# Optimization experiments

Measured on AMD Instinct MI355X. Metric: run time of the kernel, lower is better.

Reference implementation:

```python
import jax, jax.numpy as jnp
import numpy as np

B, N, D = 32, 540, 512
H = 8
DH = D // H
MAX_LEN = 540
POS_CLIP = MAX_LEN - 1


def setup_inputs() -> dict:
    key = jax.random.key(0)
    ks = jax.random.split(key, 12)
    s = 0.02
    inp = {
        "query": jax.random.normal(ks[0], (B, N, D), dtype=jnp.float32),
        "Wq": jax.random.normal(ks[1], (D, D), dtype=jnp.float32) * s,
        "bq": jnp.zeros((D,), jnp.float32),
        "Wk": jax.random.normal(ks[2], (D, D), dtype=jnp.float32) * s,
        "bk": jnp.zeros((D,), jnp.float32),
        "Wv": jax.random.normal(ks[3], (D, D), dtype=jnp.float32) * s,
        "bv": jnp.zeros((D,), jnp.float32),
        "Wh": jax.random.normal(ks[4], (D, D), dtype=jnp.float32) * s,
        "bh": jnp.zeros((D,), jnp.float32),
        "pos_k": jax.random.uniform(ks[5], (2 * POS_CLIP + 1, DH), dtype=jnp.float32, minval=-0.05, maxval=0.05),
        "gamma": jnp.ones((D,), jnp.float32),
        "beta": jnp.zeros((D,), jnp.float32),
        "valid_len": jax.random.randint(ks[6], (B,), 1, N + 1, dtype=jnp.int32),
    }
    return inp


def _split_heads(x):
    # [B, N, D] -> [H*B, N, DH], head-major on axis 0 (matches tf.concat(tf.split(x,H,-1),0))
    return x.reshape(B, N, H, DH).transpose(2, 0, 1, 3).reshape(H * B, N, DH)


def reference(query, Wq, bq, Wk, bk, Wv, bv, Wh, bh, pos_k, gamma, beta, valid_len):
    q = _split_heads(query @ Wq + bq)  # [HB, N, DH]
    k = _split_heads(query @ Wk + bk)
    v = _split_heads(query @ Wv + bv)

    QK = jnp.einsum("xqd,xkd->xqk", q, k)  # [HB, N, N]

    # relative position bias (Shaw et al. 2018)
    rel = jnp.arange(N)[None, :] - jnp.arange(N)[:, None]
    rel = jnp.clip(rel, -POS_CLIP, POS_CLIP) + POS_CLIP
    pos_enc_k = pos_k[rel]  # [N, N, DH]
    QR = jnp.einsum("xqd,qkd->xqk", q, pos_enc_k)

    attn = (QK + QR) / jnp.sqrt(jnp.float32(DH))

    # key-side sequence mask, broadcast over heads and query rows
    key_mask = jnp.arange(N)[None, :] < valid_len[:, None]  # [B, N]
    key_mask = jnp.tile(key_mask[:, None, :], (H, N, 1))  # [HB, N, N]
    attn = jnp.where(key_mask, attn, jnp.float32(-1e12))
    attn = jax.nn.softmax(attn, axis=-1)

    out = jnp.einsum("xqk,xkd->xqd", attn, v)  # [HB, N, DH]
    out = out.reshape(H, B, N, DH).transpose(1, 2, 0, 3).reshape(B, N, D)
    out = out @ Wh + bh
    out = out + query

    # layer norm over last axis
    mean = jnp.mean(out, axis=-1, keepdims=True)
    var = jnp.mean(jnp.square(out - mean), axis=-1, keepdims=True)
    normalized = (out - mean) * jax.lax.rsqrt(var + 1e-7)
    return gamma * normalized + beta
```

## Files before the change

kernel.cpp:

```cpp
#include <hip/hip_runtime.h>
#include <hip/hip_bf16.h>

typedef __hip_bfloat16 bf16;

#define NB 32
#define NSEQ 540
#define ND 512
#define NH 8
#define NDH 64
#define NHB 256
#define NM 17280
#define NPOS 1079
#define VTP 544

typedef __bf16 v8bf __attribute__((ext_vector_type(8)));
typedef float f32x4 __attribute__((ext_vector_type(4)));

union U8 {
  uint4 u;
  unsigned short s[8];
  v8bf v;
};

__device__ __forceinline__ unsigned short f2b(float x) {
  union { float f; unsigned u; } c;
  c.f = x;
  const unsigned r = c.u + 0x7fffu + ((c.u >> 16) & 1u);
  return (unsigned short)(r >> 16);
}

__device__ __forceinline__ float b2f16(unsigned short s) {
  return __uint_as_float(((unsigned)s) << 16);
}

__device__ __forceinline__ void cvt16(const float* __restrict__ p,
                                      unsigned short* __restrict__ dst) {
  unsigned short s[16];
#pragma unroll
  for (int i = 0; i < 4; i++) {
    const float4 v = *(const float4*)(p + i * 4);
    s[i * 4 + 0] = f2b(v.x);
    s[i * 4 + 1] = f2b(v.y);
    s[i * 4 + 2] = f2b(v.z);
    s[i * 4 + 3] = f2b(v.w);
  }
  *(uint4*)dst = *(uint4*)s;
  *(uint4*)(dst + 8) = *(uint4*)(s + 8);
}

__global__ __launch_bounds__(256) void pos_cvt(const float* __restrict__ pos,
                                              unsigned short* __restrict__ posb) {
  const int i = blockIdx.x * 256 + threadIdx.x;
  if (i < NPOS * NDH) posb[i] = f2b(pos[i]);
}

__global__ __launch_bounds__(256) void xcvt(const float* __restrict__ x,
                                            unsigned short* __restrict__ xb) {
  const int i = blockIdx.x * 256 + threadIdx.x;
  const float4 a = *(const float4*)(x + (size_t)i * 8);
  const float4 b = *(const float4*)(x + (size_t)i * 8 + 4);
  unsigned short s[8];
  s[0] = f2b(a.x); s[1] = f2b(a.y); s[2] = f2b(a.z); s[3] = f2b(a.w);
  s[4] = f2b(b.x); s[5] = f2b(b.y); s[6] = f2b(b.z); s[7] = f2b(b.w);
  *(uint4*)(xb + (size_t)i * 8) = *(uint4*)s;
}

__global__ __launch_bounds__(256) void wcvt(
    const float* __restrict__ Wq, const float* __restrict__ Wk,
    const float* __restrict__ Wv, const float* __restrict__ Wh,
    unsigned short* __restrict__ Wt) {
  __shared__ unsigned short T[64][72];
  const int tid = threadIdx.x;
  const int sel = blockIdx.z;
  const float* W = (sel == 0) ? Wq : (sel == 1) ? Wk : (sel == 2) ? Wv : Wh;
  unsigned short* out = Wt + (size_t)sel * ND * ND;
  const int k0 = blockIdx.x * 64, n0 = blockIdx.y * 64;
  const int r = tid >> 2, g = tid & 3;
  cvt16(W + (size_t)(k0 + r) * ND + n0 + g * 16, &T[r][g * 16]);
  __syncthreads();
  unsigned short s[16];
#pragma unroll
  for (int j = 0; j < 16; j++) s[j] = T[g * 16 + j][r];
  unsigned short* dst = out + (size_t)(n0 + r) * ND + k0 + g * 16;
  *(uint4*)dst = *(uint4*)s;
  *(uint4*)(dst + 8) = *(uint4*)(s + 8);
}

#define GEMM_MFMA_TAIL                                                            \
    __syncthreads();                                                              \
    U8 af[4], bfr[4];                                                             \
    _Pragma("unroll")                                                             \
    for (int mi = 0; mi < 4; mi++)                                                \
      af[mi].u = *(const uint4*)&As[wr * 64 + mi * 16 + l15][quad * 8];           \
    _Pragma("unroll")                                                             \
    for (int ni = 0; ni < 4; ni++)                                                \
      bfr[ni].u = *(const uint4*)&Bs[wc * 64 + ni * 16 + l15][quad * 8];          \
    _Pragma("unroll")                                                             \
    for (int mi = 0; mi < 4; mi++)                                                \
      _Pragma("unroll")                                                           \
      for (int ni = 0; ni < 4; ni++)                                              \
        acc[mi][ni] = __builtin_amdgcn_mfma_f32_16x16x32_bf16(                    \
            af[mi].v, bfr[ni].v, acc[mi][ni], 0, 0, 0);

#define GEMM_CORE_B16(APTR)                                                       \
  for (int k0 = 0; k0 < 512; k0 += 32) {                                          \
    __syncthreads();                                                              \
    {                                                                             \
      const unsigned short* apb = APTR + (size_t)(m0 + srow) * ND + k0 + sh;      \
      *(uint4*)&As[srow][sh] = *(const uint4*)apb;                                \
      *(uint4*)&As[srow][sh + 8] = *(const uint4*)(apb + 8);                      \
      const unsigned short* bp = Bt + (size_t)(n0 + srow) * ND + k0 + sh;         \
      *(uint4*)&Bs[srow][sh] = *(const uint4*)bp;                                 \
      *(uint4*)&Bs[srow][sh + 8] = *(const uint4*)(bp + 8);                       \
    }                                                                             \
    GEMM_MFMA_TAIL                                                                \
  }

#define GEMM_CORE_F32(APTR)                                                       \
  for (int k0 = 0; k0 < 512; k0 += 32) {                                          \
    __syncthreads();                                                              \
    cvt16(APTR + (size_t)(m0 + srow) * ND + k0 + sh, &As[srow][sh]);              \
    {                                                                             \
      const unsigned short* bp = Bt + (size_t)(n0 + srow) * ND + k0 + sh;         \
      *(uint4*)&Bs[srow][sh] = *(const uint4*)bp;                                 \
      *(uint4*)&Bs[srow][sh + 8] = *(const uint4*)(bp + 8);                       \
    }                                                                             \
    GEMM_MFMA_TAIL                                                                \
  }

__global__ __launch_bounds__(256, 3) void qkv_mfma(
    const unsigned short* __restrict__ Xb, const unsigned short* __restrict__ Wt,
    const float* __restrict__ bq, const float* __restrict__ bk,
    const float* __restrict__ bv,
    bf16* __restrict__ qh, bf16* __restrict__ kh, bf16* __restrict__ vt) {
  __shared__ unsigned short As[128][40];
  __shared__ unsigned short Bs[128][40];
  const int tid = threadIdx.x;
  const int sel = blockIdx.z;
  const unsigned short* Bt = Wt + (size_t)sel * ND * ND;
  const float* bias = (sel == 0) ? bq : (sel == 1) ? bk : bv;
  const int m0 = blockIdx.y * 128, n0 = blockIdx.x * 128;
  const int lane = tid & 63, w = tid >> 6;
  const int wr = w & 1, wc = w >> 1;
  const int l15 = lane & 15, quad = lane >> 4;
  const int srow = tid >> 1, sh = (tid & 1) * 16;

  f32x4 acc[4][4];
#pragma unroll
  for (int mi = 0; mi < 4; mi++)
#pragma unroll
    for (int ni = 0; ni < 4; ni++) acc[mi][ni] = (f32x4){0.f, 0.f, 0.f, 0.f};

  GEMM_CORE_B16(Xb)

  if (sel != 2) {
    unsigned short* o = (unsigned short*)((sel == 0) ? qh : kh);
#pragma unroll
    for (int mi = 0; mi < 4; mi++) {
      const int m = m0 + wr * 64 + mi * 16 + quad * 4;
      const int bidx = m / NSEQ;
      const int seq0 = m - bidx * NSEQ;
#pragma unroll
      for (int ni = 0; ni < 4; ni++) {
        const int n = n0 + wc * 64 + ni * 16 + l15;
        const int h = n >> 6, dh = n & 63;
        const float bsv = bias[n];
        const size_t base = (((size_t)(h * NB + bidx)) * NSEQ + seq0) * NDH + dh;
#pragma unroll
        for (int i = 0; i < 4; i++)
          o[base + (size_t)i * NDH] = f2b(acc[mi][ni][i] + bsv);
      }
    }
  } else {
    unsigned short* o = (unsigned short*)vt;
#pragma unroll
    for (int mi = 0; mi < 4; mi++) {
      const int m = m0 + wr * 64 + mi * 16 + quad * 4;
      const int bidx = m / NSEQ;
      const int seq0 = m - bidx * NSEQ;
#pragma unroll
      for (int ni = 0; ni < 4; ni++) {
        const int n = n0 + wc * 64 + ni * 16 + l15;
        const int h = n >> 6, dh = n & 63;
        const float bsv = bias[n];
        unsigned short pk[4];
#pragma unroll
        for (int i = 0; i < 4; i++) pk[i] = f2b(acc[mi][ni][i] + bsv);
        *(uint2*)(o + (((size_t)(h * NB + bidx)) * NDH + dh) * VTP + seq0) =
            *(uint2*)pk;
      }
    }
  }
}

__global__ __launch_bounds__(256, 3) void out_mfma(
    const float* __restrict__ ctx, const unsigned short* __restrict__ Wht,
    const float* __restrict__ bh, const float* __restrict__ query,
    float* __restrict__ tmp) {
  __shared__ unsigned short As[128][40];
  __shared__ unsigned short Bs[128][40];
  const int tid = threadIdx.x;
  const unsigned short* Bt = Wht;
  const int m0 = blockIdx.y * 128, n0 = blockIdx.x * 128;
  const int lane = tid & 63, w = tid >> 6;
  const int wr = w & 1, wc = w >> 1;
  const int l15 = lane & 15, quad = lane >> 4;
  const int srow = tid >> 1, sh = (tid & 1) * 16;

  f32x4 acc[4][4];
#pragma unroll
  for (int mi = 0; mi < 4; mi++)
#pragma unroll
    for (int ni = 0; ni < 4; ni++) acc[mi][ni] = (f32x4){0.f, 0.f, 0.f, 0.f};

  GEMM_CORE_F32(ctx)

#pragma unroll
  for (int mi = 0; mi < 4; mi++) {
    const int m = m0 + wr * 64 + mi * 16 + quad * 4;
#pragma unroll
    for (int ni = 0; ni < 4; ni++) {
      const int n = n0 + wc * 64 + ni * 16 + l15;
      const float bsv = bh[n];
#pragma unroll
      for (int i = 0; i < 4; i++) {
        const size_t off = (size_t)(m + i) * ND + n;
        tmp[off] = acc[mi][ni][i] + bsv + query[off];
      }
    }
  }
}

#define PW 584

__global__ __launch_bounds__(256, 5) void attn(
    const bf16* __restrict__ qh, const bf16* __restrict__ kh,
    const bf16* __restrict__ vt, const unsigned short* __restrict__ posb,
    const int* __restrict__ vlen, float* __restrict__ ctx) {
  __shared__ unsigned short P[16][PW];
  __shared__ float Tt[2][16][84];
  __shared__ float red4[16][4];
  __shared__ float sinv[16];

  const int tid = threadIdx.x;
  const int lane = tid & 63;
  const int w = tid >> 6;
  const int l15 = lane & 15;
  const int quad = lane >> 4;
  const int qb = blockIdx.x;
  const int x = blockIdx.y;
  const int b = x & 31, h = x >> 5;
  const int q0 = qb * 16;
  const int valid = vlen[b];
  const int NT = (valid + 63) >> 6;
  const int NC = (valid + 31) >> 5;
  const bf16* qbase = qh + (size_t)x * NSEQ * NDH;
  const unsigned short* kbase = (const unsigned short*)(kh + (size_t)x * NSEQ * NDH);
  const unsigned short* vbase = (const unsigned short*)(vt + (size_t)x * NDH * VTP);

  U8 aq0, aq1;
  {
    const int q = q0 + l15;
    if (q < NSEQ) {
      aq0.u = *(const uint4*)(qbase + (size_t)q * NDH + quad * 8);
      aq1.u = *(const uint4*)(qbase + (size_t)q * NDH + 32 + quad * 8);
    } else {
      aq0.u = make_uint4(0, 0, 0, 0);
      aq1.u = make_uint4(0, 0, 0, 0);
    }
  }

  U8 ck0, ck1, cp0, cp1, ce0, ce1;
  {
    const int key = w * 16 + l15;
    ck0.u = *(const uint4*)(kbase + (size_t)key * NDH + quad * 8);
    ck1.u = *(const uint4*)(kbase + (size_t)key * NDH + 32 + quad * 8);
    const long pr = (long)(524 - q0 + w * 16 + l15);
    cp0.u = *(const uint4*)(posb + pr * NDH + quad * 8);
    cp1.u = *(const uint4*)(posb + pr * NDH + 32 + quad * 8);
    if (w == 0) {
      const long pr2 = (long)(524 - q0 + 64 + l15);
      ce0.u = *(const uint4*)(posb + pr2 * NDH + quad * 8);
      ce1.u = *(const uint4*)(posb + pr2 * NDH + 32 + quad * 8);
    }
  }

  float pmax[4];
#pragma unroll
  for (int i = 0; i < 4; i++) pmax[i] = -1e30f;

  for (int kt = 0; kt < NT; kt++) {
    const int buf = kt & 1;
    U8 nk0, nk1, np0, np1, ne0, ne1;
    if (kt < NT - 1) {
      const int k1 = kt * 64 + 64;
      const int key = k1 + w * 16 + l15;
      nk0.u = *(const uint4*)(kbase + (size_t)key * NDH + quad * 8);
      nk1.u = *(const uint4*)(kbase + (size_t)key * NDH + 32 + quad * 8);
      const long pr = (long)(k1 - q0 + 524 + w * 16 + l15);
      np0.u = *(const uint4*)(posb + pr * NDH + quad * 8);
      np1.u = *(const uint4*)(posb + pr * NDH + 32 + quad * 8);
      if (w == 0) {
        const long pr2 = (long)(k1 - q0 + 524 + 64 + l15);
        ne0.u = *(const uint4*)(posb + pr2 * NDH + quad * 8);
        ne1.u = *(const uint4*)(posb + pr2 * NDH + 32 + quad * 8);
      }
    }

    f32x4 accqk = {0.f, 0.f, 0.f, 0.f};
    accqk = __builtin_amdgcn_mfma_f32_16x16x32_bf16(aq0.v, ck0.v, accqk, 0, 0, 0);
    accqk = __builtin_amdgcn_mfma_f32_16x16x32_bf16(aq1.v, ck1.v, accqk, 0, 0, 0);
    {
      f32x4 accT = {0.f, 0.f, 0.f, 0.f};
      accT = __builtin_amdgcn_mfma_f32_16x16x32_bf16(aq0.v, cp0.v, accT, 0, 0, 0);
      accT = __builtin_amdgcn_mfma_f32_16x16x32_bf16(aq1.v, cp1.v, accT, 0, 0, 0);
#pragma unroll
      for (int i = 0; i < 4; i++) Tt[buf][quad * 4 + i][w * 16 + l15] = accT[i];
      if (w == 0) {
        f32x4 accT2 = {0.f, 0.f, 0.f, 0.f};
        accT2 = __builtin_amdgcn_mfma_f32_16x16x32_bf16(aq0.v, ce0.v, accT2, 0, 0, 0);
        accT2 = __builtin_amdgcn_mfma_f32_16x16x32_bf16(aq1.v, ce1.v, accT2, 0, 0, 0);
#pragma unroll
        for (int i = 0; i < 4; i++) Tt[buf][quad * 4 + i][64 + l15] = accT2[i];
      }
    }
    __syncthreads();
    {
      const int k0 = kt * 64;
      const int kk = w * 16 + l15;
      const bool cm = (k0 + kk) < valid;
#pragma unroll
      for (int i = 0; i < 4; i++) {
        const int qq = quad * 4 + i;
        const float v = (accqk[i] + Tt[buf][qq][kk + 15 - qq]) * 0.125f;
        P[qq][k0 + kk] = f2b(v);
        if (cm) pmax[i] = fmaxf(pmax[i], v);
      }
    }
    ck0 = nk0; ck1 = nk1; cp0 = np0; cp1 = np1;
    if (w == 0) { ce0 = ne0; ce1 = ne1; }
  }

#pragma unroll
  for (int m = 1; m < 16; m <<= 1) {
#pragma unroll
    for (int i = 0; i < 4; i++)
      pmax[i] = fmaxf(pmax[i], __shfl_xor(pmax[i], m, 16));
  }
  if (l15 == 0) {
#pragma unroll
    for (int i = 0; i < 4; i++) red4[quad * 4 + i][w] = pmax[i];
  }

  const int dh = w * 16 + l15;
  const unsigned short* vrow = vbase + (size_t)dh * VTP;
  U8 cv;
  cv.u = *(const uint4*)(vrow + quad * 8);

  __syncthreads();

  {
    const int r = tid >> 4, c = tid & 15;
    const float4 rm = *(const float4*)red4[r];
    const float rowmax = fmaxf(fmaxf(rm.x, rm.y), fmaxf(rm.z, rm.w));
    const int nv = (valid + 7) >> 3;
    float sl = 0.f;
    for (int ch = c; ch < nv; ch += 16) {
      const uint4 u = *(const uint4*)&P[r][ch * 8];
      unsigned ue[4];
#pragma unroll
      for (int jj = 0; jj < 4; jj++) {
        const unsigned uu = ((const unsigned*)&u)[jj];
        const float lo = __uint_as_float(uu << 16);
        const float hi = __uint_as_float(uu & 0xffff0000u);
        float el = __expf(lo - rowmax);
        float eh = __expf(hi - rowmax);
        const int cb = ch * 8 + jj * 2;
        el = (cb < valid) ? el : 0.f;
        eh = (cb + 1 < valid) ? eh : 0.f;
        sl += el + eh;
        ue[jj] = (unsigned)f2b(el) | ((unsigned)f2b(eh) << 16);
      }
      *(uint4*)&P[r][ch * 8] = *(const uint4*)ue;
    }
    for (int ch = c; ch < 72; ch += 16) {
      if (ch >= nv) *(uint4*)&P[r][ch * 8] = make_uint4(0, 0, 0, 0);
    }
#pragma unroll
    for (int m = 1; m < 16; m <<= 1) sl += __shfl_xor(sl, m, 16);
    if (c == 0) sinv[r] = 1.f / sl;
  }
  __syncthreads();

  f32x4 acco = {0.f, 0.f, 0.f, 0.f};
  for (int ci = 0; ci < NC; ci++) {
    U8 nv_;
    if (ci + 1 < NC) nv_.u = *(const uint4*)(vrow + (ci + 1) * 32 + quad * 8);
    U8 ap;
    ap.u = *(const uint4*)&P[l15][ci * 32 + quad * 8];
    acco = __builtin_amdgcn_mfma_f32_16x16x32_bf16(ap.v, cv.v, acco, 0, 0, 0);
    cv = nv_;
  }
#pragma unroll
  for (int i = 0; i < 4; i++) {
    const int q = q0 + quad * 4 + i;
    if (q < NSEQ) {
      ctx[((size_t)b * NSEQ + q) * ND + h * NDH + dh] = acco[i] * sinv[quad * 4 + i];
    }
  }
}

__global__ __launch_bounds__(256) void lnorm(
    const float* __restrict__ tmp, const float* __restrict__ gamma,
    const float* __restrict__ beta, float* __restrict__ out) {
  __shared__ float sred[256];
  const int row = blockIdx.x;
  const int tid = threadIdx.x;
  const size_t base = (size_t)row * 512;
  const float x0 = tmp[base + tid];
  const float x1 = tmp[base + 256 + tid];

  sred[tid] = x0 + x1;
  __syncthreads();
  for (int o = 128; o > 0; o >>= 1) {
    if (tid < o) sred[tid] += sred[tid + o];
    __syncthreads();
  }
  const float mean = sred[0] * (1.f / 512.f);
  __syncthreads();
  const float d0 = x0 - mean, d1 = x1 - mean;
  sred[tid] = d0 * d0 + d1 * d1;
  __syncthreads();
  for (int o = 128; o > 0; o >>= 1) {
    if (tid < o) sred[tid] += sred[tid + o];
    __syncthreads();
  }
  const float var = sred[0] * (1.f / 512.f);
  const float rstd = rsqrtf(var + 1e-7f);
  out[base + tid] = d0 * rstd * gamma[tid] + beta[tid];
  out[base + 256 + tid] = d1 * rstd * gamma[tid + 256] + beta[tid + 256];
}

extern "C" void kernel_launch(void* const* d_in, const int* in_sizes, int n_in,
                              void* d_out, int out_size, void* d_ws, size_t ws_size,
                              hipStream_t stream) {
  const float* query = (const float*)d_in[0];
  const float* Wq = (const float*)d_in[1];
  const float* bq = (const float*)d_in[2];
  const float* Wk = (const float*)d_in[3];
  const float* bk = (const float*)d_in[4];
  const float* Wv = (const float*)d_in[5];
  const float* bv = (const float*)d_in[6];
  const float* Wh = (const float*)d_in[7];
  const float* bh = (const float*)d_in[8];
  const float* pos = (const float*)d_in[9];
  const float* gamma = (const float*)d_in[10];
  const float* beta = (const float*)d_in[11];
  const int* vlen = (const int*)d_in[12];

  bf16* ws = (bf16*)d_ws;
  const size_t QSZ = (size_t)NHB * NSEQ * NDH;
  const size_t VSZ = (size_t)NHB * NDH * VTP;
  bf16* qh = ws;
  bf16* kh = ws + QSZ;
  bf16* vt = ws + 2 * QSZ;
  unsigned short* posb = (unsigned short*)(ws + 2 * QSZ + VSZ);
  unsigned short* Wtb = posb + (size_t)NPOS * NDH;
  unsigned short* Xb = (unsigned short*)d_out;
  float* ctx = (float*)d_out;
  float* tmp = (float*)d_ws;
  (void)ws_size;

  pos_cvt<<<dim3(270), 256, 0, stream>>>(pos, posb);
  xcvt<<<dim3(4320), 256, 0, stream>>>(query, Xb);
  wcvt<<<dim3(8, 8, 4), 256, 0, stream>>>(Wq, Wk, Wv, Wh, Wtb);
  qkv_mfma<<<dim3(4, 135, 3), 256, 0, stream>>>(Xb, Wtb, bq, bk, bv, qh, kh, vt);
  attn<<<dim3(34, 256), 256, 0, stream>>>(qh, kh, vt, posb, vlen, ctx);
  out_mfma<<<dim3(4, 135), 256, 0, stream>>>(ctx, Wtb + 3 * (size_t)ND * ND, bh, query, tmp);
  lnorm<<<NM, 256, 0, stream>>>(tmp, gamma, beta, (float*)d_out);
}
```

Measured before the change: 333.0 us.

## Store attention context as bf16, merge prep kernels, use wave-level layernorm

The attention kernel now writes its context output as bf16 instead of fp32. The output projection can then load it directly rather than converting fp32 per tile, which halves that intermediate's memory traffic. The separate pos and x conversion kernels are merged into one launch. Layernorm now uses one wavefront per row with vectorized loads and shuffle reductions in place of a shared-memory tree with many barriers. The context is rounded to bf16 earlier than before, but the GEMM already consumed it as bf16, so accuracy should be unchanged.

```diff
diff --git a/kernel.cpp b/kernel.cpp
--- a/kernel.cpp
+++ b/kernel.cpp
@@ -48,21 +48,23 @@
   *(uint4*)(dst + 8) = *(uint4*)(s + 8);
 }
 
-__global__ __launch_bounds__(256) void pos_cvt(const float* __restrict__ pos,
-                                              unsigned short* __restrict__ posb) {
-  const int i = blockIdx.x * 256 + threadIdx.x;
-  if (i < NPOS * NDH) posb[i] = f2b(pos[i]);
-}
-
-__global__ __launch_bounds__(256) void xcvt(const float* __restrict__ x,
-                                            unsigned short* __restrict__ xb) {
-  const int i = blockIdx.x * 256 + threadIdx.x;
-  const float4 a = *(const float4*)(x + (size_t)i * 8);
-  const float4 b = *(const float4*)(x + (size_t)i * 8 + 4);
-  unsigned short s[8];
-  s[0] = f2b(a.x); s[1] = f2b(a.y); s[2] = f2b(a.z); s[3] = f2b(a.w);
-  s[4] = f2b(b.x); s[5] = f2b(b.y); s[6] = f2b(b.z); s[7] = f2b(b.w);
-  *(uint4*)(xb + (size_t)i * 8) = *(uint4*)s;
+__global__ __launch_bounds__(256) void prep(const float* __restrict__ x,
+                                            unsigned short* __restrict__ xb,
+                                            const float* __restrict__ pos,
+                                            unsigned short* __restrict__ posb) {
+  const int blk = blockIdx.x;
+  if (blk < 4320) {
+    const int i = blk * 256 + threadIdx.x;
+    const float4 a = *(const float4*)(x + (size_t)i * 8);
+    const float4 b = *(const float4*)(x + (size_t)i * 8 + 4);
+    unsigned short s[8];
+    s[0] = f2b(a.x); s[1] = f2b(a.y); s[2] = f2b(a.z); s[3] = f2b(a.w);
+    s[4] = f2b(b.x); s[5] = f2b(b.y); s[6] = f2b(b.z); s[7] = f2b(b.w);
+    *(uint4*)(xb + (size_t)i * 8) = *(uint4*)s;
+  } else {
+    const int i = (blk - 4320) * 256 + threadIdx.x;
+    if (i < NPOS * NDH) posb[i] = f2b(pos[i]);
+  }
 }
 
 __global__ __launch_bounds__(256) void wcvt(
@@ -86,7 +88,17 @@
   *(uint4*)(dst + 8) = *(uint4*)(s + 8);
 }
 
-#define GEMM_MFMA_TAIL                                                            \
+#define GEMM_CORE_B16(APTR)                                                       \
+  for (int k0 = 0; k0 < 512; k0 += 32) {                                          \
+    __syncthreads();                                                              \
+    {                                                                             \
+      const unsigned short* apb = APTR + (size_t)(m0 + srow) * ND + k0 + sh;      \
+      *(uint4*)&As[srow][sh] = *(const uint4*)apb;                                \
+      *(uint4*)&As[srow][sh + 8] = *(const uint4*)(apb + 8);                      \
+      const unsigned short* bp = Bt + (size_t)(n0 + srow) * ND + k0 + sh;         \
+      *(uint4*)&Bs[srow][sh] = *(const uint4*)bp;                                 \
+      *(uint4*)&Bs[srow][sh + 8] = *(const uint4*)(bp + 8);                       \
+    }                                                                             \
     __syncthreads();                                                              \
     U8 af[4], bfr[4];                                                             \
     _Pragma("unroll")                                                             \
@@ -100,32 +112,7 @@
       _Pragma("unroll")                                                           \
       for (int ni = 0; ni < 4; ni++)                                              \
         acc[mi][ni] = __builtin_amdgcn_mfma_f32_16x16x32_bf16(                    \
-            af[mi].v, bfr[ni].v, acc[mi][ni], 0, 0, 0);
-
-#define GEMM_CORE_B16(APTR)                                                       \
-  for (int k0 = 0; k0 < 512; k0 += 32) {                                          \
-    __syncthreads();                                                              \
-    {                                                                             \
-      const unsigned short* apb = APTR + (size_t)(m0 + srow) * ND + k0 + sh;      \
-      *(uint4*)&As[srow][sh] = *(const uint4*)apb;                                \
-      *(uint4*)&As[srow][sh + 8] = *(const uint4*)(apb + 8);                      \
-      const unsigned short* bp = Bt + (size_t)(n0 + srow) * ND + k0 + sh;         \
-      *(uint4*)&Bs[srow][sh] = *(const uint4*)bp;                                 \
-      *(uint4*)&Bs[srow][sh + 8] = *(const uint4*)(bp + 8);                       \
-    }                                                                             \
-    GEMM_MFMA_TAIL                                                                \
-  }
-
-#define GEMM_CORE_F32(APTR)                                                       \
-  for (int k0 = 0; k0 < 512; k0 += 32) {                                          \
-    __syncthreads();                                                              \
-    cvt16(APTR + (size_t)(m0 + srow) * ND + k0 + sh, &As[srow][sh]);              \
-    {                                                                             \
-      const unsigned short* bp = Bt + (size_t)(n0 + srow) * ND + k0 + sh;         \
-      *(uint4*)&Bs[srow][sh] = *(const uint4*)bp;                                 \
-      *(uint4*)&Bs[srow][sh + 8] = *(const uint4*)(bp + 8);                       \
-    }                                                                             \
-    GEMM_MFMA_TAIL                                                                \
+            af[mi].v, bfr[ni].v, acc[mi][ni], 0, 0, 0);                           \
   }
 
 __global__ __launch_bounds__(256, 3) void qkv_mfma(
@@ -194,7 +181,7 @@
 }
 
 __global__ __launch_bounds__(256, 3) void out_mfma(
-    const float* __restrict__ ctx, const unsigned short* __restrict__ Wht,
+    const unsigned short* __restrict__ ctxb, const unsigned short* __restrict__ Wht,
     const float* __restrict__ bh, const float* __restrict__ query,
     float* __restrict__ tmp) {
   __shared__ unsigned short As[128][40];
@@ -213,7 +200,7 @@
 #pragma unroll
     for (int ni = 0; ni < 4; ni++) acc[mi][ni] = (f32x4){0.f, 0.f, 0.f, 0.f};
 
-  GEMM_CORE_F32(ctx)
+  GEMM_CORE_B16(ctxb)
 
 #pragma unroll
   for (int mi = 0; mi < 4; mi++) {
@@ -236,7 +223,7 @@
 __global__ __launch_bounds__(256, 5) void attn(
     const bf16* __restrict__ qh, const bf16* __restrict__ kh,
     const bf16* __restrict__ vt, const unsigned short* __restrict__ posb,
-    const int* __restrict__ vlen, float* __restrict__ ctx) {
+    const int* __restrict__ vlen, bf16* __restrict__ ctx) {
   __shared__ unsigned short P[16][PW];
   __shared__ float Tt[2][16][84];
   __shared__ float red4[16][4];
@@ -401,11 +388,13 @@
     acco = __builtin_amdgcn_mfma_f32_16x16x32_bf16(ap.v, cv.v, acco, 0, 0, 0);
     cv = nv_;
   }
+  unsigned short* ob = (unsigned short*)ctx;
 #pragma unroll
   for (int i = 0; i < 4; i++) {
     const int q = q0 + quad * 4 + i;
     if (q < NSEQ) {
-      ctx[((size_t)b * NSEQ + q) * ND + h * NDH + dh] = acco[i] * sinv[quad * 4 + i];
+      ob[((size_t)b * NSEQ + q) * ND + h * NDH + dh] =
+          f2b(acco[i] * sinv[quad * 4 + i]);
     }
   }
 }
@@ -413,32 +402,42 @@
 __global__ __launch_bounds__(256) void lnorm(
     const float* __restrict__ tmp, const float* __restrict__ gamma,
     const float* __restrict__ beta, float* __restrict__ out) {
-  __shared__ float sred[256];
-  const int row = blockIdx.x;
-  const int tid = threadIdx.x;
-  const size_t base = (size_t)row * 512;
-  const float x0 = tmp[base + tid];
-  const float x1 = tmp[base + 256 + tid];
-
-  sred[tid] = x0 + x1;
-  __syncthreads();
-  for (int o = 128; o > 0; o >>= 1) {
-    if (tid < o) sred[tid] += sred[tid + o];
-    __syncthreads();
-  }
-  const float mean = sred[0] * (1.f / 512.f);
-  __syncthreads();
-  const float d0 = x0 - mean, d1 = x1 - mean;
-  sred[tid] = d0 * d0 + d1 * d1;
-  __syncthreads();
-  for (int o = 128; o > 0; o >>= 1) {
-    if (tid < o) sred[tid] += sred[tid + o];
-    __syncthreads();
-  }
-  const float var = sred[0] * (1.f / 512.f);
-  const float rstd = rsqrtf(var + 1e-7f);
-  out[base + tid] = d0 * rstd * gamma[tid] + beta[tid];
-  out[base + 256 + tid] = d1 * rstd * gamma[tid + 256] + beta[tid + 256];
+  const int w = threadIdx.x >> 6, lane = threadIdx.x & 63;
+  const int row = blockIdx.x * 4 + w;
+  const size_t base = (size_t)row * 512 + lane * 8;
+  const float4 a = *(const float4*)(tmp + base);
+  const float4 b = *(const float4*)(tmp + base + 4);
+
+  float s = a.x + a.y + a.z + a.w + b.x + b.y + b.z + b.w;
+#pragma unroll
+  for (int m = 1; m < 64; m <<= 1) s += __shfl_xor(s, m, 64);
+  const float mean = s * (1.f / 512.f);
+
+  float d[8] = {a.x - mean, a.y - mean, a.z - mean, a.w - mean,
+                b.x - mean, b.y - mean, b.z - mean, b.w - mean};
+  float v = 0.f;
+#pragma unroll
+  for (int i = 0; i < 8; i++) v += d[i] * d[i];
+#pragma unroll
+  for (int m = 1; m < 64; m <<= 1) v += __shfl_xor(v, m, 64);
+  const float rstd = rsqrtf(v * (1.f / 512.f) + 1e-7f);
+
+  const int col = lane * 8;
+  const float4 g0 = *(const float4*)(gamma + col);
+  const float4 g1 = *(const float4*)(gamma + col + 4);
+  const float4 be0 = *(const float4*)(beta + col);
+  const float4 be1 = *(const float4*)(beta + col + 4);
+  float4 o0, o1;
+  o0.x = d[0] * rstd * g0.x + be0.x;
+  o0.y = d[1] * rstd * g0.y + be0.y;
+  o0.z = d[2] * rstd * g0.z + be0.z;
+  o0.w = d[3] * rstd * g0.w + be0.w;
+  o1.x = d[4] * rstd * g1.x + be1.x;
+  o1.y = d[5] * rstd * g1.y + be1.y;
+  o1.z = d[6] * rstd * g1.z + be1.z;
+  o1.w = d[7] * rstd * g1.w + be1.w;
+  *(float4*)(out + base) = o0;
+  *(float4*)(out + base + 4) = o1;
 }
 
 extern "C" void kernel_launch(void* const* d_in, const int* in_sizes, int n_in,
@@ -467,15 +466,15 @@
   unsigned short* posb = (unsigned short*)(ws + 2 * QSZ + VSZ);
   unsigned short* Wtb = posb + (size_t)NPOS * NDH;
   unsigned short* Xb = (unsigned short*)d_out;
-  float* ctx = (float*)d_out;
+  bf16* ctx = (bf16*)d_out;
   float* tmp = (float*)d_ws;
   (void)ws_size;
 
-  pos_cvt<<<dim3(270), 256, 0, stream>>>(pos, posb);
-  xcvt<<<dim3(4320), 256, 0, stream>>>(query, Xb);
+  prep<<<dim3(4590), 256, 0, stream>>>(query, Xb, pos, posb);
   wcvt<<<dim3(8, 8, 4), 256, 0, stream>>>(Wq, Wk, Wv, Wh, Wtb);
   qkv_mfma<<<dim3(4, 135, 3), 256, 0, stream>>>(Xb, Wtb, bq, bk, bv, qh, kh, vt);
   attn<<<dim3(34, 256), 256, 0, stream>>>(qh, kh, vt, posb, vlen, ctx);
-  out_mfma<<<dim3(4, 135), 256, 0, stream>>>(ctx, Wtb + 3 * (size_t)ND * ND, bh, query, tmp);
-  lnorm<<<NM, 256, 0, stream>>>(tmp, gamma, beta, (float*)d_out);
-}
+  out_mfma<<<dim3(4, 135), 256, 0, stream>>>((const unsigned short*)ctx,
+                                             Wtb + 3 * (size_t)ND * ND, bh, query, tmp);
+  lnorm<<<dim3(4320), 256, 0, stream>>>(tmp, gamma, beta, (float*)d_out);
+}
```

Measured after the change: 320.6 us. -3.7%, faster.
